# Kernel optimization log

Hardware: AMD Instinct MI355X
Metric: run time of the kernel (lower is better)

## Reference

```python
import jax, jax.numpy as jnp
import numpy as np

B = 4096      # batch
F = 26        # sparse fields
V = 100000    # vocab per field
D = 64        # emb_dim
A = 64        # att_vector
ND = 13       # dense features
FEA = ND + D  # 77, BN / DNN input width
HID = [FEA, 256, 128, 64]
EPS = 1e-5


def setup_inputs() -> dict:
    key = jax.random.key(0)
    ks = jax.random.split(key, 20)
    s = 0.05  # matches .normal_(0, 0.05) init
    inp = {
        "sx": jax.random.randint(ks[0], (B, F), 0, V),
        "dx": jax.random.normal(ks[1], (B, ND), dtype=jnp.float32),
        "emb_table": jax.random.normal(ks[2], (F, V, D), dtype=jnp.float32) * s,
        "att_w_W": jax.random.normal(ks[3], (D, A), dtype=jnp.float32) * s,
        "att_w_b": jnp.zeros((A,), jnp.float32),
        "att_d_W": jax.random.normal(ks[4], (A, 1), dtype=jnp.float32) * s,
        "att_d_b": jnp.zeros((1,), jnp.float32),
        "bn_gamma": jnp.ones((FEA,), jnp.float32),
        "bn_beta": jnp.zeros((FEA,), jnp.float32),
        "w1": jax.random.normal(ks[5], (HID[0], HID[1]), dtype=jnp.float32) * s,
        "b1": jnp.zeros((HID[1],), jnp.float32),
        "w2": jax.random.normal(ks[6], (HID[1], HID[2]), dtype=jnp.float32) * s,
        "b2": jnp.zeros((HID[2],), jnp.float32),
        "w3": jax.random.normal(ks[7], (HID[2], HID[3]), dtype=jnp.float32) * s,
        "b3": jnp.zeros((HID[3],), jnp.float32),
        "wf": jax.random.normal(ks[8], (HID[3], 1), dtype=jnp.float32) * s,
        "bf": jnp.zeros((1,), jnp.float32),
    }
    return inp


def _afm_forward(sx, dx, emb_table, att_w_W, att_w_b, att_d_W, att_d_b,
                 bn_gamma, bn_beta, w1, b1, w2, b2, w3, b3, wf, bf):
    # embedding gather: [B, F, D]
    embeds = emb_table[jnp.arange(F)[None, :], sx]
    # all pairwise field interactions (upper-triangular pairs)
    i1, i2 = np.triu_indices(F, k=1)          # P = F*(F-1)/2 = 325
    bi = embeds[:, i1, :] * embeds[:, i2, :]  # [B, P, D]
    # attention MLP + softmax-weighted sum pooling over pairs
    a = jax.nn.relu(jnp.einsum("bpd,da->bpa", bi, att_w_W) + att_w_b)
    scores = jnp.einsum("bpa,ao->bpo", a, att_d_W) + att_d_b  # [B, P, 1]
    w = jax.nn.softmax(scores, axis=1)
    att_out = jnp.sum(w * bi, axis=1)         # [B, D]
    # concat with dense, batchnorm (training-mode batch stats, biased var)
    x = jnp.concatenate([att_out, dx], axis=-1)  # [B, FEA]
    mu = jnp.mean(x, axis=0)
    var = jnp.mean((x - mu) ** 2, axis=0)
    x = (x - mu) * jax.lax.rsqrt(var + EPS) * bn_gamma + bn_beta
    # DNN tower (dropout=0.0 -> identity) + final linear + sigmoid
    x = jax.nn.relu(x @ w1 + b1)
    x = jax.nn.relu(x @ w2 + b2)
    x = jax.nn.relu(x @ w3 + b3)
    out = jax.nn.sigmoid(x @ wf + bf)
    return jnp.squeeze(out, axis=-1)          # [B]


def reference(sx, dx, emb_table, att_w_W, att_w_b, att_d_W, att_d_b,
              bn_gamma, bn_beta, w1, b1, w2, b2, w3, b3, wf, bf):
    return _afm_forward(sx, dx, emb_table, att_w_W, att_w_b, att_d_W, att_d_b,
                        bn_gamma, bn_beta, w1, b1, w2, b2, w3, b3, wf, bf)
```

## Files before the change

### kernel.cpp

```cpp
#include <hip/hip_runtime.h>
#include <hip/hip_bf16.h>
#include <math.h>

#define BSZ   4096
#define F     26
#define VOC   100000
#define D     64
#define AD    64
#define ND    13
#define FEA   77
#define NPAIR 325
#define NPAD  336
#define MT    21
#define EP    68
#define H1    256
#define H2    128
#define H3    64
#define EPSF  1e-5f
#define MROW  4

typedef __attribute__((ext_vector_type(8))) short short8;
typedef __attribute__((ext_vector_type(4))) float f32x4;

union FragU { short8 s; unsigned int u[4]; };

__device__ __forceinline__ unsigned int pk2bf(float a, float b) {
  __hip_bfloat162 h = __float22bfloat162_rn(make_float2(a, b));
  return *reinterpret_cast<unsigned int*>(&h);
}
__device__ __forceinline__ unsigned short f2bf(float f) {
  unsigned int u = __float_as_uint(f);
  u += 0x7fffu + ((u >> 16) & 1u);
  return (unsigned short)(u >> 16);
}
template<int CTRL>
__device__ __forceinline__ float dpp_add(float x) {
  int xi = __builtin_bit_cast(int, x);
  int yi = __builtin_amdgcn_update_dpp(xi, xi, CTRL, 0xf, 0xf, false);
  return x + __builtin_bit_cast(float, yi);
}
__device__ __forceinline__ float row16_sum(float x) {
  x = dpp_add<0xB1>(x);
  x = dpp_add<0x4E>(x);
  x = dpp_add<0x124>(x);
  x = dpp_add<0x128>(x);
  return x;
}
__device__ __forceinline__ float bcast_lane(float v, int l) {
  return __builtin_bit_cast(float,
      __builtin_amdgcn_readlane(__builtin_bit_cast(int, v), l));
}

__global__ __launch_bounds__(256, 4) void k_attn(
    const int* __restrict__ sx, const float* __restrict__ dx,
    const float* __restrict__ emb, const float* __restrict__ attW,
    const float* __restrict__ attb, const float* __restrict__ attdW,
    const float* __restrict__ attdb, float* __restrict__ x,
    float* __restrict__ partS, float* __restrict__ partQ)
{
  __shared__ __align__(16) float e_all[4][27 * EP];
  __shared__ __align__(16) float sc_all[4][NPAD];
  __shared__ float xblk[4][80];
  __shared__ unsigned short pt[NPAD];

  const int t    = threadIdx.x;
  const int lane = t & 63;
  const int wv   = t >> 6;
  const int b    = __builtin_amdgcn_readfirstlane(blockIdx.x * 4 + wv);

  for (int p = t; p < NPAD; p += 256) {
    int f1 = 26, f2 = 26;
    if (p < NPAIR) {
      int i = 0, rem = p;
      while (rem >= F - 1 - i) { rem -= F - 1 - i; ++i; }
      f1 = i; f2 = i + 1 + rem;
    }
    pt[p] = (unsigned short)(f1 | (f2 << 8));
  }

  float* e_w  = e_all[wv];
  float* sc_w = sc_all[wv];

  {
    const int* sxb = sx + b * F;
    int rows[F];
    #pragma unroll
    for (int f = 0; f < F; ++f) rows[f] = sxb[f];
    float vf[F];
    #pragma unroll
    for (int f = 0; f < F; ++f)
      vf[f] = emb[((size_t)f * VOC + rows[f]) * D + lane];
    #pragma unroll
    for (int f = 0; f < F; ++f) e_w[f * EP + lane] = vf[f];
    e_w[26 * EP + lane] = 0.f;
  }

  short8 bfrag[2][4];
  float bj[4], dwj[4];
  {
    const int kb = (lane >> 4) * 8;
    const int cl = lane & 15;
    #pragma unroll
    for (int kk = 0; kk < 2; ++kk)
      #pragma unroll
      for (int n = 0; n < 4; ++n)
        #pragma unroll
        for (int j = 0; j < 8; ++j) {
          int k = kk * 32 + kb + j;
          bfrag[kk][n][j] = (short)f2bf(attW[k * AD + n * 16 + cl]);
        }
    #pragma unroll
    for (int n = 0; n < 4; ++n) {
      bj[n]  = attb[n * 16 + cl];
      dwj[n] = attdW[n * 16 + cl];
    }
  }
  const float db0 = attdb[0];

  __syncthreads();

  const int row16 = lane & 15;
  const int kgrp  = lane >> 4;
  const int k0    = kgrp * 8;
  for (int m = 0; m < MT; ++m) {
    const int prow = m * 16 + row16;
    const unsigned short pp = pt[prow];
    const float* r1 = &e_w[(pp & 0xff) * EP];
    const float* r2 = &e_w[(pp >> 8) * EP];
    float4 x0 = *(const float4*)&r1[k0];
    float4 x1 = *(const float4*)&r1[k0 + 4];
    float4 y0 = *(const float4*)&r2[k0];
    float4 y1 = *(const float4*)&r2[k0 + 4];
    float4 x2 = *(const float4*)&r1[32 + k0];
    float4 x3 = *(const float4*)&r1[32 + k0 + 4];
    float4 y2 = *(const float4*)&r2[32 + k0];
    float4 y3 = *(const float4*)&r2[32 + k0 + 4];
    FragU a0, a1;
    a0.u[0] = pk2bf(x0.x*y0.x, x0.y*y0.y);
    a0.u[1] = pk2bf(x0.z*y0.z, x0.w*y0.w);
    a0.u[2] = pk2bf(x1.x*y1.x, x1.y*y1.y);
    a0.u[3] = pk2bf(x1.z*y1.z, x1.w*y1.w);
    a1.u[0] = pk2bf(x2.x*y2.x, x2.y*y2.y);
    a1.u[1] = pk2bf(x2.z*y2.z, x2.w*y2.w);
    a1.u[2] = pk2bf(x3.x*y3.x, x3.y*y3.y);
    a1.u[3] = pk2bf(x3.z*y3.z, x3.w*y3.w);

    f32x4 acc[4];
    #pragma unroll
    for (int n = 0; n < 4; ++n) {
      f32x4 z = {0.f, 0.f, 0.f, 0.f};
      acc[n] = __builtin_amdgcn_mfma_f32_16x16x32_bf16(a0.s, bfrag[0][n], z, 0, 0, 0);
      acc[n] = __builtin_amdgcn_mfma_f32_16x16x32_bf16(a1.s, bfrag[1][n], acc[n], 0, 0, 0);
    }
    float v4[4];
    #pragma unroll
    for (int r = 0; r < 4; ++r) {
      float val = 0.f;
      #pragma unroll
      for (int n = 0; n < 4; ++n)
        val += fmaxf(acc[n][r] + bj[n], 0.f) * dwj[n];
      v4[r] = row16_sum(val) + db0;
    }
    if (row16 == 0) {
      float4 o = {v4[0], v4[1], v4[2], v4[3]};
      *(float4*)&sc_w[m * 16 + kgrp * 4] = o;
    }
  }

  float sv[6], ev[6];
  float mx = -1e30f;
  #pragma unroll
  for (int i = 0; i < 6; ++i) {
    int idx = lane + 64 * i;
    sv[i] = (idx < NPAIR) ? sc_w[idx] : -1e30f;
    mx = fmaxf(mx, sv[i]);
  }
  #pragma unroll
  for (int off = 32; off; off >>= 1) mx = fmaxf(mx, __shfl_xor(mx, off));
  float s = 0.f;
  #pragma unroll
  for (int i = 0; i < 6; ++i) {
    int idx = lane + 64 * i;
    ev[i] = (idx < NPAIR) ? __expf(sv[i] - mx) : 0.f;
    s += ev[i];
  }
  #pragma unroll
  for (int off = 32; off; off >>= 1) s += __shfl_xor(s, off);
  const float invZ = 1.f / s;

  float ef[F];
  #pragma unroll
  for (int f = 0; f < F; ++f) ef[f] = e_w[f * EP + lane];

  float pa0 = 0.f, pa1 = 0.f, pa2 = 0.f, pa3 = 0.f;
  {
    int p = 0;
    #pragma unroll
    for (int f1 = 0; f1 < F - 1; ++f1) {
      #pragma unroll
      for (int f2 = f1 + 1; f2 < F; ++f2) {
        const float w = bcast_lane(ev[p >> 6], p & 63);
        const float prod = ef[f1] * ef[f2];
        if ((p & 3) == 0)      pa0 = fmaf(w, prod, pa0);
        else if ((p & 3) == 1) pa1 = fmaf(w, prod, pa1);
        else if ((p & 3) == 2) pa2 = fmaf(w, prod, pa2);
        else                   pa3 = fmaf(w, prod, pa3);
        ++p;
      }
    }
  }
  const float att = ((pa0 + pa1) + (pa2 + pa3)) * invZ;

  x[(size_t)b * FEA + lane] = att;
  xblk[wv][lane] = att;
  if (lane < ND) {
    float dv = dx[b * ND + lane];
    x[(size_t)b * FEA + D + lane] = dv;
    xblk[wv][D + lane] = dv;
  }
  __syncthreads();

  if (t < FEA) {
    float x0 = xblk[0][t], x1 = xblk[1][t], x2 = xblk[2][t], x3 = xblk[3][t];
    float sS = (x0 + x1) + (x2 + x3);
    float sQ = (x0 * x0 + x1 * x1) + (x2 * x2 + x3 * x3);
    const int bkt = (blockIdx.x & 7) * 80 + t;
    atomicAdd(&partS[bkt], sS);
    atomicAdd(&partQ[bkt], sQ);
  }
}

__global__ __launch_bounds__(256) void k_mlp(
    const float* __restrict__ x,
    const float* __restrict__ partS, const float* __restrict__ partQ,
    const float* __restrict__ gamma, const float* __restrict__ beta,
    const float* __restrict__ w1, const float* __restrict__ b1,
    const float* __restrict__ w2, const float* __restrict__ b2,
    const float* __restrict__ w3, const float* __restrict__ b3,
    const float* __restrict__ wf, const float* __restrict__ bf,
    float* __restrict__ out)
{
  __shared__ float scs[80], shs[80];
  __shared__ float xn[MROW][80];
  __shared__ float h1s[MROW][H1];
  __shared__ float h2s[MROW][H2];
  __shared__ float h3s[MROW][H3];
  const int t = threadIdx.x;
  const int b0 = blockIdx.x * MROW;

  if (t < FEA) {
    float S = 0.f, Q = 0.f;
    #pragma unroll
    for (int k = 0; k < 8; ++k) {
      S += partS[k * 80 + t];
      Q += partQ[k * 80 + t];
    }
    float mu  = S * (1.f / BSZ);
    float var = Q * (1.f / BSZ) - mu * mu;
    float scl = gamma[t] * rsqrtf(var + EPSF);
    scs[t] = scl;
    shs[t] = beta[t] - mu * scl;
  }
  __syncthreads();

  for (int k = t; k < MROW * FEA; k += 256) {
    int r = k / FEA, f = k % FEA;
    xn[r][f] = x[(size_t)(b0 + r) * FEA + f] * scs[f] + shs[f];
  }
  __syncthreads();

  {
    float acc[MROW];
    const float bb = b1[t];
    #pragma unroll
    for (int r = 0; r < MROW; ++r) acc[r] = bb;
    for (int d0 = 0; d0 < FEA; d0 += 11) {
      float wl[11];
      #pragma unroll
      for (int u = 0; u < 11; ++u) wl[u] = w1[(d0 + u) * H1 + t];
      #pragma unroll
      for (int u = 0; u < 11; ++u)
        #pragma unroll
        for (int r = 0; r < MROW; ++r)
          acc[r] = fmaf(xn[r][d0 + u], wl[u], acc[r]);
    }
    #pragma unroll
    for (int r = 0; r < MROW; ++r) h1s[r][t] = fmaxf(acc[r], 0.f);
  }
  __syncthreads();

  {
    const int j = t & 127;
    const int rb = (t >> 7) * 2;
    float acc0 = b2[j], acc1 = acc0;
    for (int c0 = 0; c0 < H1; c0 += 16) {
      float wl[16];
      #pragma unroll
      for (int u = 0; u < 16; ++u) wl[u] = w2[(c0 + u) * H2 + j];
      #pragma unroll
      for (int u = 0; u < 16; ++u) {
        acc0 = fmaf(h1s[rb + 0][c0 + u], wl[u], acc0);
        acc1 = fmaf(h1s[rb + 1][c0 + u], wl[u], acc1);
      }
    }
    h2s[rb + 0][j] = fmaxf(acc0, 0.f);
    h2s[rb + 1][j] = fmaxf(acc1, 0.f);
  }
  __syncthreads();

  {
    const int j = t & 63;
    const int r = t >> 6;
    float acc = b3[j];
    for (int c0 = 0; c0 < H2; c0 += 16) {
      float wl[16];
      #pragma unroll
      for (int u = 0; u < 16; ++u) wl[u] = w3[(c0 + u) * H3 + j];
      #pragma unroll
      for (int u = 0; u < 16; ++u)
        acc = fmaf(h2s[r][c0 + u], wl[u], acc);
    }
    h3s[r][j] = fmaxf(acc, 0.f);
  }
  __syncthreads();

  if (t < MROW * 8) {
    const int r = t >> 3;
    const int g = t & 7;
    float acc = 0.f;
    #pragma unroll
    for (int u = 0; u < 8; ++u)
      acc = fmaf(h3s[r][g * 8 + u], wf[g * 8 + u], acc);
    acc = dpp_add<0xB1>(acc);
    acc = dpp_add<0x4E>(acc);
    acc = dpp_add<0x124>(acc);
    if (g == 0)
      out[b0 + r] = 1.f / (1.f + __expf(-(acc + bf[0])));
  }
}

extern "C" void kernel_launch(void* const* d_in, const int* in_sizes, int n_in,
                              void* d_out, int out_size, void* d_ws, size_t ws_size,
                              hipStream_t stream) {
  const int*   sx    = (const int*)  d_in[0];
  const float* dx    = (const float*)d_in[1];
  const float* emb   = (const float*)d_in[2];
  const float* attW  = (const float*)d_in[3];
  const float* attb  = (const float*)d_in[4];
  const float* attdW = (const float*)d_in[5];
  const float* attdb = (const float*)d_in[6];
  const float* gamma = (const float*)d_in[7];
  const float* beta  = (const float*)d_in[8];
  const float* w1    = (const float*)d_in[9];
  const float* b1    = (const float*)d_in[10];
  const float* w2    = (const float*)d_in[11];
  const float* b2    = (const float*)d_in[12];
  const float* w3    = (const float*)d_in[13];
  const float* b3    = (const float*)d_in[14];
  const float* wf    = (const float*)d_in[15];
  const float* bf    = (const float*)d_in[16];
  float* out = (float*)d_out;

  float* x     = (float*)d_ws;
  float* partS = x + (size_t)BSZ * FEA;
  float* partQ = partS + 8 * 80;

  hipMemsetAsync(partS, 0, 2 * 8 * 80 * sizeof(float), stream);
  k_attn<<<BSZ / 4, 256, 0, stream>>>(sx, dx, emb, attW, attb, attdW, attdb,
                                      x, partS, partQ);
  k_mlp<<<BSZ / MROW, 256, 0, stream>>>(x, partS, partQ, gamma, beta,
                                        w1, b1, w2, b2, w3, b3, wf, bf, out);
}
```

Before: 65.08 us.

## Use lane broadcasts instead of shared memory in MLP; vectorize attention epilogue

The MLP kernel now holds the normalized inputs and hidden activations in registers and reads them through cross-lane broadcasts (bcast_lane) rather than staging xn/h3 in shared memory. This removes two barriers, and the final layer becomes one wave per row with a shuffle reduction. The attention loop is rewritten with vector multiply, max and FMA on f32x4. This is meant to cut LDS traffic and barrier cost, at the price of many readlane/permute operations. bcast_lane must already exist in the hidden part of the code.

```diff
diff --git a/kernel.cpp b/kernel.cpp
--- a/kernel.cpp
+++ b/kernel.cpp
@@ -17,7 +17,6 @@
 #define H2    128
 #define H3    64
 #define EPSF  1e-5f
-#define MROW  4
 
 typedef __attribute__((ext_vector_type(8))) short short8;
 typedef __attribute__((ext_vector_type(4))) float f32x4;
@@ -122,47 +121,48 @@
   const int row16 = lane & 15;
   const int kgrp  = lane >> 4;
   const int k0    = kgrp * 8;
+  const f32x4 zero4 = {0.f, 0.f, 0.f, 0.f};
   for (int m = 0; m < MT; ++m) {
     const int prow = m * 16 + row16;
     const unsigned short pp = pt[prow];
     const float* r1 = &e_w[(pp & 0xff) * EP];
     const float* r2 = &e_w[(pp >> 8) * EP];
-    float4 x0 = *(const float4*)&r1[k0];
-    float4 x1 = *(const float4*)&r1[k0 + 4];
-    float4 y0 = *(const float4*)&r2[k0];
-    float4 y1 = *(const float4*)&r2[k0 + 4];
-    float4 x2 = *(const float4*)&r1[32 + k0];
-    float4 x3 = *(const float4*)&r1[32 + k0 + 4];
-    float4 y2 = *(const float4*)&r2[32 + k0];
-    float4 y3 = *(const float4*)&r2[32 + k0 + 4];
+    f32x4 xv0 = *(const f32x4*)&r1[k0];
+    f32x4 xv1 = *(const f32x4*)&r1[k0 + 4];
+    f32x4 yv0 = *(const f32x4*)&r2[k0];
+    f32x4 yv1 = *(const f32x4*)&r2[k0 + 4];
+    f32x4 xv2 = *(const f32x4*)&r1[32 + k0];
+    f32x4 xv3 = *(const f32x4*)&r1[32 + k0 + 4];
+    f32x4 yv2 = *(const f32x4*)&r2[32 + k0];
+    f32x4 yv3 = *(const f32x4*)&r2[32 + k0 + 4];
+    f32x4 pa = xv0 * yv0;
+    f32x4 pb = xv1 * yv1;
+    f32x4 pc = xv2 * yv2;
+    f32x4 pd = xv3 * yv3;
     FragU a0, a1;
-    a0.u[0] = pk2bf(x0.x*y0.x, x0.y*y0.y);
-    a0.u[1] = pk2bf(x0.z*y0.z, x0.w*y0.w);
-    a0.u[2] = pk2bf(x1.x*y1.x, x1.y*y1.y);
-    a0.u[3] = pk2bf(x1.z*y1.z, x1.w*y1.w);
-    a1.u[0] = pk2bf(x2.x*y2.x, x2.y*y2.y);
-    a1.u[1] = pk2bf(x2.z*y2.z, x2.w*y2.w);
-    a1.u[2] = pk2bf(x3.x*y3.x, x3.y*y3.y);
-    a1.u[3] = pk2bf(x3.z*y3.z, x3.w*y3.w);
+    a0.u[0] = pk2bf(pa[0], pa[1]); a0.u[1] = pk2bf(pa[2], pa[3]);
+    a0.u[2] = pk2bf(pb[0], pb[1]); a0.u[3] = pk2bf(pb[2], pb[3]);
+    a1.u[0] = pk2bf(pc[0], pc[1]); a1.u[1] = pk2bf(pc[2], pc[3]);
+    a1.u[2] = pk2bf(pd[0], pd[1]); a1.u[3] = pk2bf(pd[2], pd[3]);
 
     f32x4 acc[4];
     #pragma unroll
     for (int n = 0; n < 4; ++n) {
-      f32x4 z = {0.f, 0.f, 0.f, 0.f};
-      acc[n] = __builtin_amdgcn_mfma_f32_16x16x32_bf16(a0.s, bfrag[0][n], z, 0, 0, 0);
+      acc[n] = __builtin_amdgcn_mfma_f32_16x16x32_bf16(a0.s, bfrag[0][n], zero4, 0, 0, 0);
       acc[n] = __builtin_amdgcn_mfma_f32_16x16x32_bf16(a1.s, bfrag[1][n], acc[n], 0, 0, 0);
     }
-    float v4[4];
-    #pragma unroll
-    for (int r = 0; r < 4; ++r) {
-      float val = 0.f;
-      #pragma unroll
-      for (int n = 0; n < 4; ++n)
-        val += fmaxf(acc[n][r] + bj[n], 0.f) * dwj[n];
-      v4[r] = row16_sum(val) + db0;
-    }
+    f32x4 vale = zero4;
+    #pragma unroll
+    for (int n = 0; n < 4; ++n) {
+      f32x4 rl = __builtin_elementwise_max(acc[n] + bj[n], zero4);
+      vale = rl * dwj[n] + vale;
+    }
+    float s0 = row16_sum(vale[0]) + db0;
+    float s1 = row16_sum(vale[1]) + db0;
+    float s2 = row16_sum(vale[2]) + db0;
+    float s3 = row16_sum(vale[3]) + db0;
     if (row16 == 0) {
-      float4 o = {v4[0], v4[1], v4[2], v4[3]};
+      float4 o = {s0, s1, s2, s3};
       *(float4*)&sc_w[m * 16 + kgrp * 4] = o;
     }
   }
@@ -240,102 +240,137 @@
     const float* __restrict__ wf, const float* __restrict__ bf,
     float* __restrict__ out)
 {
-  __shared__ float scs[80], shs[80];
-  __shared__ float xn[MROW][80];
-  __shared__ float h1s[MROW][H1];
-  __shared__ float h2s[MROW][H2];
-  __shared__ float h3s[MROW][H3];
-  const int t = threadIdx.x;
-  const int b0 = blockIdx.x * MROW;
-
-  if (t < FEA) {
-    float S = 0.f, Q = 0.f;
+  __shared__ float h1s[4][H1];
+  __shared__ float h2s[4][H2];
+  const int t    = threadIdx.x;
+  const int lane = t & 63;
+  const int wvid = t >> 6;
+  const int b0   = blockIdx.x * 4;
+
+  float scl0, sh0, scl1 = 0.f, sh1 = 0.f;
+  {
+    float S0 = 0.f, Q0 = 0.f;
     #pragma unroll
     for (int k = 0; k < 8; ++k) {
-      S += partS[k * 80 + t];
-      Q += partQ[k * 80 + t];
-    }
-    float mu  = S * (1.f / BSZ);
-    float var = Q * (1.f / BSZ) - mu * mu;
-    float scl = gamma[t] * rsqrtf(var + EPSF);
-    scs[t] = scl;
-    shs[t] = beta[t] - mu * scl;
+      S0 += partS[k * 80 + lane];
+      Q0 += partQ[k * 80 + lane];
+    }
+    float mu0  = S0 * (1.f / BSZ);
+    float var0 = Q0 * (1.f / BSZ) - mu0 * mu0;
+    scl0 = gamma[lane] * rsqrtf(var0 + EPSF);
+    sh0  = beta[lane] - mu0 * scl0;
+    if (lane < ND) {
+      float S1 = 0.f, Q1 = 0.f;
+      #pragma unroll
+      for (int k = 0; k < 8; ++k) {
+        S1 += partS[k * 80 + 64 + lane];
+        Q1 += partQ[k * 80 + 64 + lane];
+      }
+      float mu1  = S1 * (1.f / BSZ);
+      float var1 = Q1 * (1.f / BSZ) - mu1 * mu1;
+      scl1 = gamma[64 + lane] * rsqrtf(var1 + EPSF);
+      sh1  = beta[64 + lane] - mu1 * scl1;
+    }
+  }
+
+  float xa[4], xb[4];
+  #pragma unroll
+  for (int r = 0; r < 4; ++r) {
+    xa[r] = x[(size_t)(b0 + r) * FEA + lane] * scl0 + sh0;
+    xb[r] = (lane < ND) ? x[(size_t)(b0 + r) * FEA + 64 + lane] * scl1 + sh1 : 0.f;
+  }
+
+  {
+    float acc[4];
+    const float bb = b1[t];
+    #pragma unroll
+    for (int r = 0; r < 4; ++r) acc[r] = bb;
+    #pragma unroll
+    for (int d0 = 0; d0 < 72; d0 += 8) {
+      float wl[8];
+      #pragma unroll
+      for (int u = 0; u < 8; ++u) wl[u] = w1[(d0 + u) * H1 + t];
+      #pragma unroll
+      for (int u = 0; u < 8; ++u) {
+        const int d = d0 + u;
+        #pragma unroll
+        for (int r = 0; r < 4; ++r) {
+          const float sv = (d < 64) ? bcast_lane(xa[r], d) : bcast_lane(xb[r], d - 64);
+          acc[r] = fmaf(sv, wl[u], acc[r]);
+        }
+      }
+    }
+    {
+      float wl[5];
+      #pragma unroll
+      for (int u = 0; u < 5; ++u) wl[u] = w1[(72 + u) * H1 + t];
+      #pragma unroll
+      for (int u = 0; u < 5; ++u) {
+        #pragma unroll
+        for (int r = 0; r < 4; ++r) {
+          const float sv = bcast_lane(xb[r], 8 + u);
+          acc[r] = fmaf(sv, wl[u], acc[r]);
+        }
+      }
+    }
+    #pragma unroll
+    for (int r = 0; r < 4; ++r) h1s[r][t] = fmaxf(acc[r], 0.f);
   }
   __syncthreads();
 
-  for (int k = t; k < MROW * FEA; k += 256) {
-    int r = k / FEA, f = k % FEA;
-    xn[r][f] = x[(size_t)(b0 + r) * FEA + f] * scs[f] + shs[f];
+  const int j2 = t & 127;
+  const int rb = (t >> 7) * 2;
+  {
+    float h1a[4], h1b[4];
+    #pragma unroll
+    for (int k = 0; k < 4; ++k) {
+      h1a[k] = h1s[rb + 0][lane + 64 * k];
+      h1b[k] = h1s[rb + 1][lane + 64 * k];
+    }
+    float acc0 = b2[j2], acc1 = acc0;
+    #pragma unroll
+    for (int c0 = 0; c0 < H1; c0 += 8) {
+      float wl[8];
+      #pragma unroll
+      for (int u = 0; u < 8; ++u) wl[u] = w2[(c0 + u) * H2 + j2];
+      #pragma unroll
+      for (int u = 0; u < 8; ++u) {
+        const int c = c0 + u;
+        acc0 = fmaf(bcast_lane(h1a[c >> 6], c & 63), wl[u], acc0);
+        acc1 = fmaf(bcast_lane(h1b[c >> 6], c & 63), wl[u], acc1);
+      }
+    }
+    h2s[rb + 0][j2] = fmaxf(acc0, 0.f);
+    h2s[rb + 1][j2] = fmaxf(acc1, 0.f);
   }
   __syncthreads();
 
-  {
-    float acc[MROW];
-    const float bb = b1[t];
-    #pragma unroll
-    for (int r = 0; r < MROW; ++r) acc[r] = bb;
-    for (int d0 = 0; d0 < FEA; d0 += 11) {
-      float wl[11];
-      #pragma unroll
-      for (int u = 0; u < 11; ++u) wl[u] = w1[(d0 + u) * H1 + t];
-      #pragma unroll
-      for (int u = 0; u < 11; ++u)
-        #pragma unroll
-        for (int r = 0; r < MROW; ++r)
-          acc[r] = fmaf(xn[r][d0 + u], wl[u], acc[r]);
-    }
-    #pragma unroll
-    for (int r = 0; r < MROW; ++r) h1s[r][t] = fmaxf(acc[r], 0.f);
-  }
-  __syncthreads();
-
-  {
-    const int j = t & 127;
-    const int rb = (t >> 7) * 2;
-    float acc0 = b2[j], acc1 = acc0;
-    for (int c0 = 0; c0 < H1; c0 += 16) {
-      float wl[16];
-      #pragma unroll
-      for (int u = 0; u < 16; ++u) wl[u] = w2[(c0 + u) * H2 + j];
-      #pragma unroll
-      for (int u = 0; u < 16; ++u) {
-        acc0 = fmaf(h1s[rb + 0][c0 + u], wl[u], acc0);
-        acc1 = fmaf(h1s[rb + 1][c0 + u], wl[u], acc1);
-      }
-    }
-    h2s[rb + 0][j] = fmaxf(acc0, 0.f);
-    h2s[rb + 1][j] = fmaxf(acc1, 0.f);
-  }
-  __syncthreads();
-
-  {
-    const int j = t & 63;
-    const int r = t >> 6;
-    float acc = b3[j];
-    for (int c0 = 0; c0 < H2; c0 += 16) {
-      float wl[16];
-      #pragma unroll
-      for (int u = 0; u < 16; ++u) wl[u] = w3[(c0 + u) * H3 + j];
-      #pragma unroll
-      for (int u = 0; u < 16; ++u)
-        acc = fmaf(h2s[r][c0 + u], wl[u], acc);
-    }
-    h3s[r][j] = fmaxf(acc, 0.f);
-  }
-  __syncthreads();
-
-  if (t < MROW * 8) {
-    const int r = t >> 3;
-    const int g = t & 7;
-    float acc = 0.f;
-    #pragma unroll
-    for (int u = 0; u < 8; ++u)
-      acc = fmaf(h3s[r][g * 8 + u], wf[g * 8 + u], acc);
-    acc = dpp_add<0xB1>(acc);
-    acc = dpp_add<0x4E>(acc);
-    acc = dpp_add<0x124>(acc);
-    if (g == 0)
-      out[b0 + r] = 1.f / (1.f + __expf(-(acc + bf[0])));
+  float h3v;
+  {
+    float h2a[2];
+    h2a[0] = h2s[wvid][lane];
+    h2a[1] = h2s[wvid][64 + lane];
+    float acc = b3[lane];
+    #pragma unroll
+    for (int c0 = 0; c0 < H2; c0 += 8) {
+      float wl[8];
+      #pragma unroll
+      for (int u = 0; u < 8; ++u) wl[u] = w3[(c0 + u) * H3 + lane];
+      #pragma unroll
+      for (int u = 0; u < 8; ++u) {
+        const int c = c0 + u;
+        acc = fmaf(bcast_lane(h2a[c >> 6], c & 63), wl[u], acc);
+      }
+    }
+    h3v = fmaxf(acc, 0.f);
+  }
+
+  {
+    float v = h3v * wf[lane];
+    #pragma unroll
+    for (int off = 32; off; off >>= 1) v += __shfl_xor(v, off);
+    if (lane == 0)
+      out[b0 + wvid] = 1.f / (1.f + __expf(-(v + bf[0])));
   }
 }
 
@@ -368,6 +403,6 @@
   hipMemsetAsync(partS, 0, 2 * 8 * 80 * sizeof(float), stream);
   k_attn<<<BSZ / 4, 256, 0, stream>>>(sx, dx, emb, attW, attb, attdW, attdb,
                                       x, partS, partQ);
-  k_mlp<<<BSZ / MROW, 256, 0, stream>>>(x, partS, partQ, gamma, beta,
-                                        w1, b1, w2, b2, w3, b3, wf, bf, out);
-}
+  k_mlp<<<BSZ / 4, 256, 0, stream>>>(x, partS, partQ, gamma, beta,
+                                     w1, b1, w2, b2, w3, b3, wf, bf, out);
+}
```

Result: slower. 70.67 us (+8.6%).
